# Kernel tuning notes

Hardware: AMD Instinct MI355X
Metric: run time of the kernel (lower is better)

The kernel has to match this reference:

```python
import jax, jax.numpy as jnp
import numpy as np

N = 12000   # nodes (multiple of 120)
E = 192000  # edges
T = 120     # utterances per dialogue
IN = 192
OUT = 6


def _edge_softmax(logits, dst, n):
    # logits: [E, H] -> softmax over incoming edges of each dst node
    m = jax.ops.segment_max(logits, dst, num_segments=n)
    ex = jnp.exp(logits - m[dst])
    s = jax.ops.segment_sum(ex, dst, num_segments=n)
    return ex / s[dst]


def _gatv2(h, src, dst, Wsrc, bsrc, Wdst, bdst, attn, Wres, n):
    # DGL GATv2Conv: e = attn . leakyrelu(fc_src(h)[u] + fc_dst(h)[v]), residual, relu activation
    Hh, F = attn.shape
    fs = (h @ Wsrc + bsrc).reshape(n, Hh, F)
    fd = (h @ Wdst + bdst).reshape(n, Hh, F)
    e = jax.nn.leaky_relu(fs[src] + fd[dst], 0.2)          # [E, H, F]
    logits = jnp.einsum('ehf,hf->eh', e, attn)              # [E, H]
    alpha = _edge_softmax(logits, dst, n)                   # [E, H]
    out = jax.ops.segment_sum(alpha[:, :, None] * fs[src], dst, num_segments=n)
    res = (h @ Wres).reshape(n, Hh, F)
    return jax.nn.relu(out + res)                           # [N, H, F]


def _lstm_dir(x, Wih, Whh, bih, bhh, reverse):
    # x: [T, B, D]; torch gate order i, f, g, o
    B = x.shape[1]
    hid = Whh.shape[1]
    def step(carry, xt):
        h, c = carry
        z = xt @ Wih.T + h @ Whh.T + bih + bhh
        i, f, g, o = jnp.split(z, 4, axis=-1)
        c = jax.nn.sigmoid(f) * c + jax.nn.sigmoid(i) * jnp.tanh(g)
        h = jax.nn.sigmoid(o) * jnp.tanh(c)
        return (h, c), h
    init = (jnp.zeros((B, hid), x.dtype), jnp.zeros((B, hid), x.dtype))
    _, hs = jax.lax.scan(step, init, x, reverse=reverse)
    return hs


def setup_inputs() -> dict:
    key = jax.random.key(0)
    ks = iter(jax.random.split(key, 64))
    def rn(shape, s=0.05):
        return jax.random.normal(next(ks), shape, jnp.float32) * s
    inp = {
        'text': rn((N, 1024), 1.0),
        'audio': rn((N, 512), 1.0),
        'vision': rn((N, 1024), 1.0),
        'edge_src': jax.random.randint(next(ks), (E,), 0, N, jnp.int32),
        'edge_dst': jax.random.randint(next(ks), (E,), 0, N, jnp.int32),
        # modality encoders
        'W_audio': rn((512, 64)), 'b_audio': jnp.zeros((64,), jnp.float32),
        'W_vision': rn((1024, 64)), 'b_vision': jnp.zeros((64,), jnp.float32),
        'W_text': rn((1024, 64)), 'b_text': jnp.zeros((64,), jnp.float32),
        # bidirectional LSTM (hidden=4 -> 16 gate rows)
        'Wih_f': rn((16, IN)), 'Whh_f': rn((16, 4)), 'bih_f': jnp.zeros((16,), jnp.float32), 'bhh_f': jnp.zeros((16,), jnp.float32),
        'Wih_b': rn((16, IN)), 'Whh_b': rn((16, 4)), 'bih_b': jnp.zeros((16,), jnp.float32), 'bhh_b': jnp.zeros((16,), jnp.float32),
        # imputation GraphConv (192->192, norm='both')
        'W_gc': rn((IN, IN)), 'b_gc': jnp.zeros((IN,), jnp.float32),
        # gat2 (cross-modal multi-head GAT, 192 -> 16 heads x 4)
        'Wsrc2': rn((IN, 64)), 'bsrc2': jnp.zeros((64,), jnp.float32),
        'Wdst2': rn((IN, 64)), 'bdst2': jnp.zeros((64,), jnp.float32),
        'attn2': rn((16, 4)), 'Wres2': rn((IN, 64)),
        # gat1 layer 0 (192 -> 16 heads x 32)
        'Wsrc0': rn((IN, 512)), 'bsrc0': jnp.zeros((512,), jnp.float32),
        'Wdst0': rn((IN, 512)), 'bdst0': jnp.zeros((512,), jnp.float32),
        'attn0': rn((16, 32)), 'Wres0': rn((IN, 512)),
        # gat1 layer 1 (512 -> 16 heads x 4)
        'Wsrc1': rn((512, 64)), 'bsrc1': jnp.zeros((64,), jnp.float32),
        'Wdst1': rn((512, 64)), 'bdst1': jnp.zeros((64,), jnp.float32),
        'attn1': rn((16, 4)), 'Wres1': rn((512, 64)),
        # final classifier Linear(136, out_size)
        'W_lin': rn((136, OUT)), 'b_lin': jnp.zeros((OUT,), jnp.float32),
    }
    return inp


def reference(text, audio, vision, edge_src, edge_dst,
              W_audio, b_audio, W_vision, b_vision, W_text, b_text,
              Wih_f, Whh_f, bih_f, bhh_f, Wih_b, Whh_b, bih_b, bhh_b,
              W_gc, b_gc,
              Wsrc2, bsrc2, Wdst2, bdst2, attn2, Wres2,
              Wsrc0, bsrc0, Wdst0, bdst0, attn0, Wres0,
              Wsrc1, bsrc1, Wdst1, bdst1, attn1, Wres1,
              W_lin, b_lin):
    n = text.shape[0]
    # modality encoders (dropout is identity at inference)
    t = text @ W_text + b_text
    a = audio @ W_audio + b_audio
    v = vision @ W_vision + b_vision
    stackFT = jnp.concatenate([t, a, v], axis=1)            # [N, 192]

    # bidirectional LSTM over dialogues of length T=120
    x = stackFT.reshape(-1, T, IN).transpose(1, 0, 2)       # [T, B, 192]
    hf = _lstm_dir(x, Wih_f, Whh_f, bih_f, bhh_f, False)
    hb = _lstm_dir(x, Wih_b, Whh_b, bih_b, bhh_b, True)
    newFeature = jnp.concatenate([hf, hb], -1).transpose(1, 0, 2).reshape(n, 8)

    # GraphConv imputation, norm='both' (degrees clamped to 1 as in DGL)
    ones = jnp.ones((edge_src.shape[0],), stackFT.dtype)
    deg_out = jnp.maximum(jax.ops.segment_sum(ones, edge_src, num_segments=n), 1.0)
    deg_in = jnp.maximum(jax.ops.segment_sum(ones, edge_dst, num_segments=n), 1.0)
    hw = (stackFT @ W_gc) * (deg_out ** -0.5)[:, None]
    h1 = jax.ops.segment_sum(hw[edge_src], edge_dst, num_segments=n) * (deg_in ** -0.5)[:, None] + b_gc
    h = 0.5 * (stackFT + h1)
    # F.normalize(h, p=1)
    h = h / jnp.maximum(jnp.sum(jnp.abs(h), axis=1, keepdims=True), 1e-12)

    # cross-modal multi-head GAT branch -> [N, 64]
    h3 = _gatv2(h, edge_src, edge_dst, Wsrc2, bsrc2, Wdst2, bdst2, attn2, Wres2, n).reshape(n, -1)

    # stacked GATv2 layers
    h = _gatv2(h, edge_src, edge_dst, Wsrc0, bsrc0, Wdst0, bdst0, attn0, Wres0, n).reshape(n, -1)  # [N, 512]
    h = _gatv2(h, edge_src, edge_dst, Wsrc1, bsrc1, Wdst1, bdst1, attn1, Wres1, n).reshape(n, -1)  # [N, 64]

    out = jnp.concatenate([h, newFeature, h3], axis=1) @ W_lin + b_lin  # [N, out_size]
    return out
```

## Files before the change

kernel.cpp:

```cpp
#include <hip/hip_runtime.h>

typedef __attribute__((ext_vector_type(8))) short short8;
typedef __attribute__((ext_vector_type(4))) float f32x4;
typedef _Float16 half8v __attribute__((ext_vector_type(8)));

__device__ __forceinline__ unsigned short f2bf(float f) {
    unsigned u = __float_as_uint(f);
    u += 0x7FFFu + ((u >> 16) & 1u);
    return (unsigned short)(u >> 16);
}
__device__ __forceinline__ float bf2f(unsigned short h) {
    return __uint_as_float((unsigned)h << 16);
}

template<int MF, int OUTMODE>
__global__ __launch_bounds__(256)
void gemm_v7(const unsigned short* __restrict__ A, const unsigned short* __restrict__ B,
             const float* __restrict__ bias, const float* __restrict__ rowscale,
             void* __restrict__ Cv, const float* __restrict__ fin_num,
             const float* __restrict__ fin_den,
             int M, int Nb, int K, int ldc)
{
    __shared__ alignas(16) unsigned short As[MF * 64 * 32];
    __shared__ alignas(16) unsigned short Bs[4 * 64 * 8];
    const int t = threadIdx.x;
    const int w = t >> 6, l = t & 63;
    const int r16 = l & 15, kg = l >> 4;
    const int row0 = blockIdx.x * (64 * MF);
    const int col0 = blockIdx.y * 64;
    const int bcol = t & 63, bkg = t >> 6;

    f32x4 acc[MF][4] = {};
    const short8 z8 = {0, 0, 0, 0, 0, 0, 0, 0};

    int srow[MF], sch[MF];
    bool va[MF];
    const unsigned short* aptr[MF];
#pragma unroll
    for (int it = 0; it < MF; ++it) {
        int idx = it * 256 + t;
        srow[it] = idx >> 2; sch[it] = idx & 3;
        int gm = row0 + srow[it];
        va[it] = gm < M;
        aptr[it] = A + (size_t)gm * K + sch[it] * 8;
    }
    const unsigned short* bptr = B + (size_t)(bkg * 8) * Nb + col0 + bcol;

    short8 pa[MF];
    unsigned short pbv[8];
#pragma unroll
    for (int it = 0; it < MF; ++it)
        pa[it] = va[it] ? *reinterpret_cast<const short8*>(aptr[it]) : z8;
#pragma unroll
    for (int j = 0; j < 8; ++j) pbv[j] = bptr[(size_t)j * Nb];

    for (int k0 = 0; k0 < K; k0 += 32) {
#pragma unroll
        for (int it = 0; it < MF; ++it)
            *reinterpret_cast<short8*>(&As[srow[it] * 32 + sch[it] * 8]) = pa[it];
        {
            short8 hv;
#pragma unroll
            for (int j = 0; j < 8; ++j) hv[j] = (short)pbv[j];
            *reinterpret_cast<short8*>(&Bs[bkg * 512 + bcol * 8]) = hv;
        }
        __syncthreads();
        if (k0 + 32 < K) {
#pragma unroll
            for (int it = 0; it < MF; ++it)
                pa[it] = va[it] ? *reinterpret_cast<const short8*>(aptr[it] + k0 + 32) : z8;
#pragma unroll
            for (int j = 0; j < 8; ++j) pbv[j] = bptr[(size_t)(k0 + 32 + j) * Nb];
        }
        short8 af[MF];
#pragma unroll
        for (int mi = 0; mi < MF; ++mi)
            af[mi] = *reinterpret_cast<const short8*>(&As[((w * MF + mi) * 16 + r16) * 32 + kg * 8]);
#pragma unroll
        for (int ni = 0; ni < 4; ++ni) {
            short8 bf = *reinterpret_cast<const short8*>(&Bs[kg * 512 + (ni * 16 + r16) * 8]);
#pragma unroll
            for (int mi = 0; mi < MF; ++mi)
                acc[mi][ni] = __builtin_amdgcn_mfma_f32_16x16x32_bf16(af[mi], bf, acc[mi][ni], 0, 0, 0);
        }
        __syncthreads();
    }
#pragma unroll
    for (int mi = 0; mi < MF; ++mi)
#pragma unroll
        for (int ni = 0; ni < 4; ++ni) {
            int col = col0 + ni * 16 + r16;
            float bv = bias ? bias[col] : 0.f;
#pragma unroll
            for (int r = 0; r < 4; ++r) {
                int gm = row0 + (w * MF + mi) * 16 + kg * 4 + r;
                if (gm < M) {
                    float val = acc[mi][ni][r] + bv;
                    if (rowscale) val *= rowscale[gm];
                    size_t idx = (size_t)gm * ldc + col;
                    if (OUTMODE == 0) {
                        ((float*)Cv)[idx] = val;
                    } else if (OUTMODE == 1) {
                        ((unsigned short*)Cv)[idx] = f2bf(val);
                    } else {
                        float d = fin_den[(size_t)gm * 16 + (col >> 5)];
                        float inv = (d > 0.f) ? __fdividef(1.f, d) : 0.f;
                        float o = fmaxf(fin_num[idx] * inv + val, 0.f);
                        ((unsigned short*)Cv)[idx] = f2bf(o);
                    }
                }
            }
        }
}

__global__ __launch_bounds__(256)
void enc_f16v2(const float* __restrict__ text, const float* __restrict__ audio, const float* __restrict__ vision,
               const _Float16* __restrict__ Wf16,
               const float* __restrict__ bt, const float* __restrict__ ba, const float* __restrict__ bv,
               float* __restrict__ Cf, unsigned short* __restrict__ Cb, int M)
{
    __shared__ alignas(16) _Float16 Af[32 * 64];
    __shared__ alignas(16) _Float16 Bf[8 * 64 * 8];
    const int z = blockIdx.z;
    const float* A  = (z == 0) ? text : (z == 1) ? audio : vision;
    const _Float16* W = Wf16 + ((z == 0) ? 0 : (z == 1) ? 65536 : 98304);
    const float* bb = (z == 0) ? bt : (z == 1) ? ba : bv;
    const int K = (z == 1) ? 512 : 1024;

    const int t = threadIdx.x;
    const int w = t >> 6, l = t & 63;
    const int r16 = l & 15, kg = l >> 4;
    const int row0 = blockIdx.x * 32;
    const int mi = w & 1;
    const int ncol0 = (w >> 1) * 32;
    const int arow = t >> 3, ac8 = t & 7;
    const int bcol = t & 63, bw = t >> 6;

    const float* ap = A + (size_t)(row0 + arow) * K + ac8 * 8;
    const _Float16* wp = W + (size_t)(bw * 16) * 64 + bcol;

    float4 pa0 = *reinterpret_cast<const float4*>(ap);
    float4 pa1 = *reinterpret_cast<const float4*>(ap + 4);
    _Float16 pb[16];
#pragma unroll
    for (int j = 0; j < 16; ++j) pb[j] = wp[(size_t)j * 64];

    f32x4 acc[2] = {};
    const int asw = ac8 ^ (arow & 7);
    for (int k0 = 0; k0 < K; k0 += 64) {
        {
            half8v av;
            av[0] = (_Float16)pa0.x; av[1] = (_Float16)pa0.y;
            av[2] = (_Float16)pa0.z; av[3] = (_Float16)pa0.w;
            av[4] = (_Float16)pa1.x; av[5] = (_Float16)pa1.y;
            av[6] = (_Float16)pa1.z; av[7] = (_Float16)pa1.w;
            *reinterpret_cast<half8v*>(&Af[arow * 64 + asw * 8]) = av;
            half8v b0, b1;
#pragma unroll
            for (int j = 0; j < 8; ++j) { b0[j] = pb[j]; b1[j] = pb[8 + j]; }
            *reinterpret_cast<half8v*>(&Bf[(bw * 2) * 512 + bcol * 8]) = b0;
            *reinterpret_cast<half8v*>(&Bf[(bw * 2 + 1) * 512 + bcol * 8]) = b1;
        }
        __syncthreads();
        if (k0 + 64 < K) {
            pa0 = *reinterpret_cast<const float4*>(ap + k0 + 64);
            pa1 = *reinterpret_cast<const float4*>(ap + k0 + 68);
#pragma unroll
            for (int j = 0; j < 16; ++j) pb[j] = wp[(size_t)(k0 + 64 + j) * 64];
        }
        const int row = mi * 16 + r16;
        half8v afA = *reinterpret_cast<const half8v*>(&Af[row * 64 + (kg ^ (row & 7)) * 8]);
        half8v afB = *reinterpret_cast<const half8v*>(&Af[row * 64 + ((kg + 4) ^ (row & 7)) * 8]);
#pragma unroll
        for (int ni = 0; ni < 2; ++ni) {
            int cx = (ncol0 + ni * 16 + r16) * 8;
            half8v bf0 = *reinterpret_cast<const half8v*>(&Bf[kg * 512 + cx]);
            half8v bf1 = *reinterpret_cast<const half8v*>(&Bf[(kg + 4) * 512 + cx]);
            acc[ni] = __builtin_amdgcn_mfma_f32_16x16x32_f16(afA, bf0, acc[ni], 0, 0, 0);
            acc[ni] = __builtin_amdgcn_mfma_f32_16x16x32_f16(afB, bf1, acc[ni], 0, 0, 0);
        }
        __syncthreads();
    }
#pragma unroll
    for (int ni = 0; ni < 2; ++ni) {
        int col = ncol0 + ni * 16 + r16;
        float bvv = bb[col];
#pragma unroll
        for (int r = 0; r < 4; ++r) {
            int gr = row0 + mi * 16 + kg * 4 + r;
            if (gr < M) {
                float val = acc[ni][r] + bvv;
                size_t idx = (size_t)gr * 192 + z * 64 + col;
                Cf[idx] = val;
                Cb[idx] = f2bf(val);
            }
        }
    }
}

__global__ void pack_all(const float* __restrict__ Wt, const float* __restrict__ Wa, const float* __restrict__ Wv,
                         const float* __restrict__ Wgc,
                         const float* __restrict__ Ws2, const float* __restrict__ Wd2, const float* __restrict__ Wr2,
                         const float* __restrict__ bs2, const float* __restrict__ bd2,
                         const float* __restrict__ Ws0, const float* __restrict__ Wd0,
                         const float* __restrict__ bs0, const float* __restrict__ bd0,
                         const float* __restrict__ Wr0,
                         const float* __restrict__ Ws1, const float* __restrict__ Wd1, const float* __restrict__ Wr1,
                         const float* __restrict__ bs1, const float* __restrict__ bd1,
                         _Float16* __restrict__ encW, unsigned short* __restrict__ Wall, float* __restrict__ ball)
{
    int gid = blockIdx.x * blockDim.x + threadIdx.x;
    if (gid < 163840) {
        float v = (gid < 65536) ? Wt[gid] : (gid < 98304) ? Wa[gid - 65536] : Wv[gid - 98304];
        encW[gid] = (_Float16)v;
    }
    if (gid < 36864) {
        Wall[gid] = f2bf(Wgc[gid]);
    } else if (gid < 73728) {
        int i = gid - 36864, k = i / 192, c = i - k * 192;
        float v = (c < 64) ? Ws2[k * 64 + c] : (c < 128) ? Wd2[k * 64 + c - 64] : Wr2[k * 64 + c - 128];
        Wall[gid] = f2bf(v);
    } else if (gid < 270336) {
        int i = gid - 73728, k = i >> 10, c = i & 1023;
        float v = (c < 512) ? Ws0[k * 512 + c] : Wd0[k * 512 + c - 512];
        Wall[gid] = f2bf(v);
    } else if (gid < 368640) {
        Wall[gid] = f2bf(Wr0[gid - 270336]);
    } else if (gid < 466944) {
        int i = gid - 368640, k = i / 192, c = i - k * 192;
        float v = (c < 64) ? Ws1[k * 64 + c] : (c < 128) ? Wd1[k * 64 + c - 64] : Wr1[k * 64 + c - 128];
        Wall[gid] = f2bf(v);
    } else if (gid < 468352) {
        int i = gid - 466944;
        float v;
        if (i < 192)       v = (i < 64) ? bs2[i] : (i < 128) ? bd2[i - 64] : 0.f;
        else if (i < 1216) { int j = i - 192; v = (j < 512) ? bs0[j] : bd0[j - 512]; }
        else               { int j = i - 1216; v = (j < 64) ? bs1[j] : (j < 128) ? bd1[j - 64] : 0.f; }
        ball[i] = v;
    }
}

__global__ void deg_kernel(const int* __restrict__ src, const int* __restrict__ dst,
                           int* degout, int* degin, int E)
{
    int e = blockIdx.x * blockDim.x + threadIdx.x;
    if (e < E) {
        atomicAdd(&degout[src[e]], 1);
        atomicAdd(&degin[dst[e]], 1);
    }
}

__global__ __launch_bounds__(1024)
void scan_kernel(const int* __restrict__ degin, int* __restrict__ rowstart, int n)
{
    __shared__ int part[1024];
    int t = threadIdx.x;
    int chunk = (n + 1023) / 1024;
    int s = 0;
    for (int i = 0; i < chunk; ++i) {
        int idx = t * chunk + i;
        if (idx < n) s += degin[idx];
    }
    part[t] = s;
    __syncthreads();
    for (int o = 1; o < 1024; o <<= 1) {
        int v = (t >= o) ? part[t - o] : 0;
        __syncthreads();
        part[t] += v;
        __syncthreads();
    }
    int run = (t > 0) ? part[t - 1] : 0;
    for (int i = 0; i < chunk; ++i) {
        int idx = t * chunk + i;
        if (idx < n) { rowstart[idx] = run; run += degin[idx]; }
    }
    if (t == 1023) rowstart[n] = part[1023];
}

__global__ void perm_kernel(const int* __restrict__ dst, const int* __restrict__ rowstart,
                            int* cursor, int* __restrict__ perm, int E)
{
    int e = blockIdx.x * blockDim.x + threadIdx.x;
    if (e < E) {
        int v = dst[e];
        int p = atomicAdd(&cursor[v], 1);
        perm[rowstart[v] + p] = e;
    }
}

__global__ void gather_src_kernel(const int* __restrict__ esrc, int* perm, int E)
{
    int i = blockIdx.x * blockDim.x + threadIdx.x;
    if (i < E) perm[i] = esrc[perm[i]];
}

__global__ void rs_kernel(const int* degout, const int* degin, float* rso, float* rsi, int n)
{
    int i = blockIdx.x * blockDim.x + threadIdx.x;
    if (i < n) {
        rso[i] = rsqrtf((float)max(degout[i], 1));
        rsi[i] = rsqrtf((float)max(degin[i], 1));
    }
}

__global__ void lstm_pre(const float* __restrict__ x, const float* __restrict__ Wf,
                         const float* __restrict__ Wb,
                         const float* bf1, const float* bf2, const float* bb1, const float* bb2,
                         float* __restrict__ xWf, float* __restrict__ xWb, int n)
{
    int gid = blockIdx.x * blockDim.x + threadIdx.x;
    if (gid >= n * 32) return;
    int nn = gid >> 5, r = gid & 31, d = r >> 4, j = r & 15;
    const float* W = (d ? Wb : Wf) + j * 192;
    const float* xr = x + (size_t)nn * 192;
    float s = 0.f;
#pragma unroll 4
    for (int k = 0; k < 192; k += 4) {
        float4 xv = *reinterpret_cast<const float4*>(xr + k);
        float4 wv = *reinterpret_cast<const float4*>(W + k);
        s += xv.x * wv.x + xv.y * wv.y + xv.z * wv.z + xv.w * wv.w;
    }
    s += d ? (bb1[j] + bb2[j]) : (bf1[j] + bf2[j]);
    int b = nn / 120, tt = nn - b * 120;
    (d ? xWb : xWf)[((size_t)b * 16 + j) * 120 + tt] = s;
}

__device__ __forceinline__ float fsigm(float x) { return __fdividef(1.f, 1.f + __expf(-x)); }
__device__ __forceinline__ float ftanh(float x) { return 1.f - __fdividef(2.f, __expf(2.f * x) + 1.f); }

template<int DIR>
__device__ void lstm_chain(const float* __restrict__ xw, const float* __restrict__ whh,
                           float* __restrict__ newF, int b)
{
    int j = threadIdx.x & 15;
    int k = j & 3;
    float4 w = *reinterpret_cast<const float4*>(whh + j * 4);
    const float* xp = xw + ((size_t)b * 16 + j) * 120;
    float h0 = 0.f, h1 = 0.f, h2 = 0.f, h3 = 0.f, cst = 0.f;
    int tb0 = DIR ? 108 : 0;
    float4 a0 = *reinterpret_cast<const float4*>(xp + tb0);
    float4 a1 = *reinterpret_cast<const float4*>(xp + tb0 + 4);
    float4 a2 = *reinterpret_cast<const float4*>(xp + tb0 + 8);
    for (int ch = 0; ch < 10; ++ch) {
        float4 b0 = a0, b1 = a1, b2 = a2;
        if (ch < 9) {
            int nt = DIR ? (96 - ch * 12) : (12 + ch * 12);
            b0 = *reinterpret_cast<const float4*>(xp + nt);
            b1 = *reinterpret_cast<const float4*>(xp + nt + 4);
            b2 = *reinterpret_cast<const float4*>(xp + nt + 8);
        }
        float zz[12] = {a0.x, a0.y, a0.z, a0.w, a1.x, a1.y, a1.z, a1.w, a2.x, a2.y, a2.z, a2.w};
        int tbase = DIR ? (108 - ch * 12) : (ch * 12);
#pragma unroll
        for (int ii = 0; ii < 12; ++ii) {
            int idx = DIR ? (11 - ii) : ii;
            float z = zz[idx] + ((w.x * h0 + w.y * h1) + (w.z * h2 + w.w * h3));
            float zi = __shfl(z, k, 16);
            float zf = __shfl(z, k + 4, 16);
            float zg = __shfl(z, k + 8, 16);
            float zo = __shfl(z, k + 12, 16);
            float ig = fsigm(zi), fg = fsigm(zf), gg = ftanh(zg), og = fsigm(zo);
            cst = fg * cst + ig * gg;
            float hn = og * ftanh(cst);
            h0 = __shfl(hn, 0, 16); h1 = __shfl(hn, 1, 16);
            h2 = __shfl(hn, 2, 16); h3 = __shfl(hn, 3, 16);
            if (j < 4) newF[((size_t)b * 120 + tbase + idx) * 8 + DIR * 4 + j] = hn;
        }
        a0 = b0; a1 = b1; a2 = b2;
    }
}

__global__ __launch_bounds__(64)
void lstm_seq2(const float* __restrict__ xWf, const float* __restrict__ xWb,
               const float* __restrict__ Whhf, const float* __restrict__ Whhb,
               float* __restrict__ newF, int B)
{
    int sub = threadIdx.x >> 4;
    int chain = blockIdx.x * 4 + sub;
    if (chain >= 2 * B) return;
    int d = chain / B;
    int b = chain - d * B;
    if (d == 0) lstm_chain<0>(xWf, Whhf, newF, b);
    else        lstm_chain<1>(xWb, Whhb, newF, b);
}

__global__ __launch_bounds__(256)
void gc_combine5(const float* __restrict__ stackFT, const unsigned short* __restrict__ hw,
                 const int* __restrict__ rowstart, const int* __restrict__ csrc,
                 const float* __restrict__ rs_in,
                 const float* __restrict__ b_gc, unsigned short* __restrict__ hB, int n)
{
    int v = blockIdx.x * 4 + (threadIdx.x >> 6);
    int l = threadIdx.x & 63;
    if (v >= n) return;
    int s0 = rowstart[v], s1 = rowstart[v + 1];
    float sum0 = 0.f, sum1 = 0.f, sum2 = 0.f;

    unsigned short a0 = 0, a1 = 0, a2 = 0, b0 = 0, b1 = 0, b2 = 0;
    auto LD = [&](int i, unsigned short& x0, unsigned short& x1, unsigned short& x2) {
        const unsigned short* hr = hw + (size_t)csrc[i] * 192 + l;
        x0 = hr[0]; x1 = hr[64]; x2 = hr[128];
    };
    int i = s0;
    if (i < s1) LD(i, a0, a1, a2);
    if (i + 1 < s1) LD(i + 1, b0, b1, b2);
    for (; i + 2 < s1; i += 2) {
        unsigned short n0, n1, n2, m0 = 0, m1 = 0, m2 = 0;
        LD(i + 2, n0, n1, n2);
        if (i + 3 < s1) LD(i + 3, m0, m1, m2);
        sum0 += bf2f(a0) + bf2f(b0);
        sum1 += bf2f(a1) + bf2f(b1);
        sum2 += bf2f(a2) + bf2f(b2);
        a0 = n0; a1 = n1; a2 = n2; b0 = m0; b1 = m1; b2 = m2;
    }
    if (i < s1) { sum0 += bf2f(a0); sum1 += bf2f(a1); sum2 += bf2f(a2); }
    if (i + 1 < s1) { sum0 += bf2f(b0); sum1 += bf2f(b1); sum2 += bf2f(b2); }

    float ri = rs_in[v];
    const float* sf = stackFT + (size_t)v * 192 + l;
    float v0 = 0.5f * (sf[0]   + sum0 * ri + b_gc[l]);
    float v1 = 0.5f * (sf[64]  + sum1 * ri + b_gc[l + 64]);
    float v2 = 0.5f * (sf[128] + sum2 * ri + b_gc[l + 128]);
    float r = fabsf(v0) + fabsf(v1) + fabsf(v2);
#pragma unroll
    for (int o = 32; o; o >>= 1) r += __shfl_xor(r, o);
    float inv = __fdividef(1.f, fmaxf(r, 1e-12f));
    unsigned short* hp = hB + (size_t)v * 192 + l;
    hp[0]   = f2bf(v0 * inv);
    hp[64]  = f2bf(v1 * inv);
    hp[128] = f2bf(v2 * inv);
}

__global__ __launch_bounds__(256)
void gat_edge4c(const unsigned short* __restrict__ base,
                const float* __restrict__ attn,
                const int* __restrict__ rowstart, const int* __restrict__ csrc,
                float* __restrict__ outp, int n)
{
    int v = blockIdx.x * 16 + (threadIdx.x >> 4);
    int l = threadIdx.x & 15;
    if (v >= n) return;
    float4 at = *reinterpret_cast<const float4*>(attn + l * 4);
    ushort4 fdu = *reinterpret_cast<const ushort4*>(base + (size_t)v * 192 + 64 + l * 4);
    float fd0 = bf2f(fdu.x), fd1 = bf2f(fdu.y), fd2 = bf2f(fdu.z), fd3 = bf2f(fdu.w);
    float ac0 = 0.f, ac1 = 0.f, ac2 = 0.f, ac3 = 0.f, dn = 0.f;
    int s0 = rowstart[v], s1 = rowstart[v + 1];

    auto LD = [&](int i) -> ushort4 {
        return *reinterpret_cast<const ushort4*>(base + (size_t)csrc[i] * 192 + l * 4);
    };
    auto ACC = [&](ushort4 su) {
        float s0f = bf2f(su.x), s1f = bf2f(su.y), s2f = bf2f(su.z), s3f = bf2f(su.w);
        float e0 = s0f + fd0; e0 = fmaxf(e0, 0.2f * e0);
        float e1 = s1f + fd1; e1 = fmaxf(e1, 0.2f * e1);
        float e2 = s2f + fd2; e2 = fmaxf(e2, 0.2f * e2);
        float e3 = s3f + fd3; e3 = fmaxf(e3, 0.2f * e3);
        float p = e0 * at.x + e1 * at.y + e2 * at.z + e3 * at.w;
        float ex = __expf(p);
        ac0 += ex * s0f; ac1 += ex * s1f; ac2 += ex * s2f; ac3 += ex * s3f;
        dn += ex;
    };
    const ushort4 zu = make_ushort4(0, 0, 0, 0);
    ushort4 c0 = zu, c1 = zu;
    int i = s0;
    if (i < s1) c0 = LD(i);
    if (i + 1 < s1) c1 = LD(i + 1);
    for (; i + 2 < s1; i += 2) {
        ushort4 n0 = LD(i + 2);
        ushort4 n1 = (i + 3 < s1) ? LD(i + 3) : zu;
        ACC(c0); ACC(c1);
        c0 = n0; c1 = n1;
    }
    if (i < s1) ACC(c0);
    if (i + 1 < s1) ACC(c1);

    ushort4 ru = *reinterpret_cast<const ushort4*>(base + (size_t)v * 192 + 128 + l * 4);
    float inv = (dn > 0.f) ? __fdividef(1.f, dn) : 0.f;
    float4 o;
    o.x = fmaxf(ac0 * inv + bf2f(ru.x), 0.f);
    o.y = fmaxf(ac1 * inv + bf2f(ru.y), 0.f);
    o.z = fmaxf(ac2 * inv + bf2f(ru.z), 0.f);
    o.w = fmaxf(ac3 * inv + bf2f(ru.w), 0.f);
    *reinterpret_cast<float4*>(outp + (size_t)v * 64 + l * 4) = o;
}

__global__ __launch_bounds__(256)
void gat_edge32b(const unsigned short* __restrict__ base,
                 const float* __restrict__ attn,
                 const int* __restrict__ rowstart, const int* __restrict__ csrc,
                 float* __restrict__ num, float* __restrict__ den, int n)
{
    int v = blockIdx.x * 4 + (threadIdx.x >> 6);
    int l = threadIdx.x & 63;
    if (v >= n) return;
    float at[8];
    {
        float4 aA = *reinterpret_cast<const float4*>(attn + l * 8);
        float4 aB = *reinterpret_cast<const float4*>(attn + l * 8 + 4);
        at[0] = aA.x; at[1] = aA.y; at[2] = aA.z; at[3] = aA.w;
        at[4] = aB.x; at[5] = aB.y; at[6] = aB.z; at[7] = aB.w;
    }
    float fd[8];
    {
        short8 fdu = *reinterpret_cast<const short8*>(base + (size_t)v * 1024 + 512 + l * 8);
#pragma unroll
        for (int j = 0; j < 8; ++j) fd[j] = bf2f((unsigned short)fdu[j]);
    }
    float acc[8] = {};
    float dn = 0.f;
    int s0 = rowstart[v], s1 = rowstart[v + 1];

    auto LD = [&](int i) -> short8 {
        return *reinterpret_cast<const short8*>(base + (size_t)csrc[i] * 1024 + l * 8);
    };
    auto ACC = [&](short8 su) {
        float sf[8];
        float p = 0.f;
#pragma unroll
        for (int j = 0; j < 8; ++j) {
            sf[j] = bf2f((unsigned short)su[j]);
            float e = sf[j] + fd[j];
            e = fmaxf(e, 0.2f * e);
            p += e * at[j];
        }
        p += __shfl_xor(p, 1, 4);
        p += __shfl_xor(p, 2, 4);
        float ex = __expf(p);
#pragma unroll
        for (int j = 0; j < 8; ++j) acc[j] += ex * sf[j];
        dn += ex;
    };
    const short8 z8 = {0, 0, 0, 0, 0, 0, 0, 0};
    short8 c0 = z8, c1 = z8;
    int i = s0;
    if (i < s1) c0 = LD(i);
    if (i + 1 < s1) c1 = LD(i + 1);
    for (; i + 2 < s1; i += 2) {
        short8 n0 = LD(i + 2);
        short8 n1 = (i + 3 < s1) ? LD(i + 3) : z8;
        ACC(c0); ACC(c1);
        c0 = n0; c1 = n1;
    }
    if (i < s1) ACC(c0);
    if (i + 1 < s1) ACC(c1);

    float* np = num + (size_t)v * 512 + l * 8;
    *reinterpret_cast<float4*>(np)     = make_float4(acc[0], acc[1], acc[2], acc[3]);
    *reinterpret_cast<float4*>(np + 4) = make_float4(acc[4], acc[5], acc[6], acc[7]);
    if ((l & 3) == 0) den[(size_t)v * 16 + (l >> 2)] = dn;
}

__global__ void final_lin(const float* __restrict__ h1, const float* __restrict__ newF,
                          const float* __restrict__ h3, const float* __restrict__ W,
                          const float* __restrict__ bias, float* __restrict__ out, int n)
{
    int gid = blockIdx.x * blockDim.x + threadIdx.x;
    if (gid >= n * 6) return;
    int v = gid / 6, o = gid - v * 6;
    float s = bias[o];
    const float* a = h1 + (size_t)v * 64;
#pragma unroll 8
    for (int r = 0; r < 64; ++r) s += a[r] * W[r * 6 + o];
    const float* b = newF + (size_t)v * 8;
#pragma unroll
    for (int r = 0; r < 8; ++r) s += b[r] * W[(64 + r) * 6 + o];
    const float* c = h3 + (size_t)v * 64;
#pragma unroll 8
    for (int r = 0; r < 64; ++r) s += c[r] * W[(72 + r) * 6 + o];
    out[gid] = s;
}

extern "C" void kernel_launch(void* const* d_in, const int* in_sizes, int n_in,
                              void* d_out, int out_size, void* d_ws, size_t ws_size,
                              hipStream_t stream)
{
    const float* text   = (const float*)d_in[0];
    const float* audio  = (const float*)d_in[1];
    const float* vision = (const float*)d_in[2];
    const int*   esrc   = (const int*)d_in[3];
    const int*   edst   = (const int*)d_in[4];
    const float* W_audio = (const float*)d_in[5];  const float* b_audio = (const float*)d_in[6];
    const float* W_vision= (const float*)d_in[7];  const float* b_vision= (const float*)d_in[8];
    const float* W_text  = (const float*)d_in[9];  const float* b_text  = (const float*)d_in[10];
    const float* Wih_f = (const float*)d_in[11]; const float* Whh_f = (const float*)d_in[12];
    const float* bih_f = (const float*)d_in[13]; const float* bhh_f = (const float*)d_in[14];
    const float* Wih_b = (const float*)d_in[15]; const float* Whh_b = (const float*)d_in[16];
    const float* bih_b = (const float*)d_in[17]; const float* bhh_b = (const float*)d_in[18];
    const float* W_gc  = (const float*)d_in[19]; const float* b_gc  = (const float*)d_in[20];
    const float* Wsrc2 = (const float*)d_in[21]; const float* bsrc2 = (const float*)d_in[22];
    const float* Wdst2 = (const float*)d_in[23]; const float* bdst2 = (const float*)d_in[24];
    const float* attn2 = (const float*)d_in[25]; const float* Wres2 = (const float*)d_in[26];
    const float* Wsrc0 = (const float*)d_in[27]; const float* bsrc0 = (const float*)d_in[28];
    const float* Wdst0 = (const float*)d_in[29]; const float* bdst0 = (const float*)d_in[30];
    const float* attn0 = (const float*)d_in[31]; const float* Wres0 = (const float*)d_in[32];
    const float* Wsrc1 = (const float*)d_in[33]; const float* bsrc1 = (const float*)d_in[34];
    const float* Wdst1 = (const float*)d_in[35]; const float* bdst1 = (const float*)d_in[36];
    const float* attn1 = (const float*)d_in[37]; const float* Wres1 = (const float*)d_in[38];
    const float* W_lin = (const float*)d_in[39]; const float* b_lin = (const float*)d_in[40];
    float* out = (float*)d_out;

    const int n = in_sizes[0] / 1024;
    const int E = in_sizes[3];
    const int B = n / 120;

    char* p = (char*)d_ws;
    auto alloc_f = [&](size_t cnt) { float* r = (float*)p; p += ((cnt * 4 + 255) / 256) * 256; return r; };
    auto alloc_h = [&](size_t cnt) { unsigned short* r = (unsigned short*)p; p += ((cnt * 2 + 255) / 256) * 256; return r; };
    auto alloc_i = [&](size_t cnt) { int* r = (int*)p; p += ((cnt * 4 + 255) / 256) * 256; return r; };
    float*          stackFT = alloc_f((size_t)n * 192);
    unsigned short* stackBF = alloc_h((size_t)n * 192);
    unsigned short* hbufBF  = alloc_h((size_t)n * 192);
    unsigned short* encW    = alloc_h(163840);
    float* xWf     = alloc_f((size_t)n * 16);
    float* xWb     = alloc_f((size_t)n * 16);
    float* newF    = alloc_f((size_t)n * 8);
    float* big0    = alloc_f((size_t)n * 512);
    float* big1    = alloc_f((size_t)n * 512);
    float* big2    = alloc_f((size_t)n * 512);
    float* den     = alloc_f((size_t)n * 16);
    float* h3      = alloc_f((size_t)n * 64);
    float* h1s     = alloc_f((size_t)n * 64);
    float* rs_out  = alloc_f(n);
    float* rs_in   = alloc_f(n);
    int* zero_base = alloc_i((size_t)3 * n);
    int* degout = zero_base;
    int* degin  = zero_base + n;
    int* cursor = zero_base + 2 * n;
    int* rowstart = alloc_i((size_t)n + 1);
    int* perm     = alloc_i((size_t)E);
    if ((size_t)(p - (char*)d_ws) > ws_size) return;

    unsigned short* Wall = (unsigned short*)h1s;
    float* ball = h1s + 240000;
    const unsigned short* Wp_gc = Wall;
    const unsigned short* Wp_g2 = Wall + 36864;
    const unsigned short* Wp_g0 = Wall + 73728;
    const unsigned short* Wp_r0 = Wall + 270336;
    const unsigned short* Wp_g1 = Wall + 368640;
    const float* bp_g2 = ball;
    const float* bp_g0 = ball + 192;
    const float* bp_g1 = ball + 1216;

    hipMemsetAsync(zero_base, 0, (size_t)3 * n * 4, stream);
    pack_all<<<(468352 + 255) / 256, 256, 0, stream>>>(
        W_text, W_audio, W_vision, W_gc,
        Wsrc2, Wdst2, Wres2, bsrc2, bdst2,
        Wsrc0, Wdst0, bsrc0, bdst0, Wres0,
        Wsrc1, Wdst1, Wres1, bsrc1, bdst1,
        (_Float16*)encW, Wall, ball);
    deg_kernel<<<(E + 255) / 256, 256, 0, stream>>>(esrc, edst, degout, degin, E);
    scan_kernel<<<1, 1024, 0, stream>>>(degin, rowstart, n);
    perm_kernel<<<(E + 255) / 256, 256, 0, stream>>>(edst, rowstart, cursor, perm, E);
    gather_src_kernel<<<(E + 255) / 256, 256, 0, stream>>>(esrc, perm, E);
    rs_kernel<<<(n + 255) / 256, 256, 0, stream>>>(degout, degin, rs_out, rs_in, n);
    const int* csrc = perm;

    auto gemm = [&](auto mf_tag, auto om_tag, const unsigned short* A, const unsigned short* Bm,
                    const float* bias, const float* rsc, void* Cp,
                    const float* fnum, const float* fden, int M, int Nb, int K, int ldc) {
        constexpr int MF = decltype(mf_tag)::value;
        constexpr int OM = decltype(om_tag)::value;
        dim3 grid((M + 64 * MF - 1) / (64 * MF), Nb / 64);
        gemm_v7<MF, OM><<<grid, 256, 0, stream>>>(A, Bm, bias, rsc, Cp, fnum, fden, M, Nb, K, ldc);
    };
    using I1 = std::integral_constant<int, 1>;
    using I2 = std::integral_constant<int, 2>;
    using O1 = std::integral_constant<int, 1>;
    using O2 = std::integral_constant<int, 2>;

    {
        dim3 grid(n / 32, 1, 3);
        enc_f16v2<<<grid, 256, 0, stream>>>(text, audio, vision, (const _Float16*)encW,
                                            b_text, b_audio, b_vision, stackFT, stackBF, n);
    }

    lstm_pre<<<(n * 32 + 255) / 256, 256, 0, stream>>>(stackFT, Wih_f, Wih_b,
                                                       bih_f, bhh_f, bih_b, bhh_b, xWf, xWb, n);
    lstm_seq2<<<(2 * B + 3) / 4, 64, 0, stream>>>(xWf, xWb, Whh_f, Whh_b, newF, B);

    gemm(I1{}, O1{}, stackBF, Wp_gc, nullptr, rs_out, big0, nullptr, nullptr, n, 192, 192, 192);
    gc_combine5<<<(n + 3) / 4, 256, 0, stream>>>(stackFT, (const unsigned short*)big0,
                                                 rowstart, csrc, rs_in, b_gc, hbufBF, n);

    gemm(I1{}, O1{}, hbufBF, Wp_g2, bp_g2, nullptr, big0, nullptr, nullptr, n, 192, 192, 192);
    gat_edge4c<<<(n + 15) / 16, 256, 0, stream>>>((const unsigned short*)big0, attn2, rowstart, csrc, h3, n);

    gemm(I2{}, O1{}, hbufBF, Wp_g0, bp_g0, nullptr, big0, nullptr, nullptr, n, 1024, 192, 1024);
    gat_edge32b<<<(n + 3) / 4, 256, 0, stream>>>((const unsigned short*)big0, attn0, rowstart, csrc, big2, den, n);
    gemm(I1{}, O2{}, hbufBF, Wp_r0, nullptr, nullptr, big1, big2, den, n, 512, 192, 512);

    gemm(I1{}, O1{}, (const unsigned short*)big1, Wp_g1, bp_g1, nullptr, big0, nullptr, nullptr, n, 192, 512, 192);
    gat_edge4c<<<(n + 15) / 16, 256, 0, stream>>>((const unsigned short*)big0, attn1, rowstart, csrc, h1s, n);

    final_lin<<<(n * 6 + 255) / 256, 256, 0, stream>>>(h1s, newF, h3, W_lin, b_lin, out, n);
}
```

Before: 344.2 us.

## Rewrite encoder GEMM as LDS-free per-wave MFMA with prepacked weight fragments

New measurement: 358.5 us. 1.04x slower.

```diff
diff --git a/kernel.cpp b/kernel.cpp
--- a/kernel.cpp
+++ b/kernel.cpp
@@ -114,86 +114,69 @@
 }
 
 __global__ __launch_bounds__(256)
-void enc_f16v2(const float* __restrict__ text, const float* __restrict__ audio, const float* __restrict__ vision,
+void enc_f16v5(const float* __restrict__ text, const float* __restrict__ audio, const float* __restrict__ vision,
                const _Float16* __restrict__ Wf16,
                const float* __restrict__ bt, const float* __restrict__ ba, const float* __restrict__ bv,
                float* __restrict__ Cf, unsigned short* __restrict__ Cb, int M)
 {
-    __shared__ alignas(16) _Float16 Af[32 * 64];
-    __shared__ alignas(16) _Float16 Bf[8 * 64 * 8];
-    const int z = blockIdx.z;
+    const int gw = (blockIdx.x * blockDim.x + threadIdx.x) >> 6;
+    const int l = threadIdx.x & 63;
+    const int tpm = M >> 4;
+    if (gw >= 3 * tpm) return;
+    const int z = gw / tpm;
+    const int tile = gw - z * tpm;
     const float* A  = (z == 0) ? text : (z == 1) ? audio : vision;
-    const _Float16* W = Wf16 + ((z == 0) ? 0 : (z == 1) ? 65536 : 98304);
+    const _Float16* Wp = Wf16 + ((z == 0) ? 0 : (z == 1) ? 65536 : 98304) + l * 8;
     const float* bb = (z == 0) ? bt : (z == 1) ? ba : bv;
-    const int K = (z == 1) ? 512 : 1024;
-
-    const int t = threadIdx.x;
-    const int w = t >> 6, l = t & 63;
-    const int r16 = l & 15, kg = l >> 4;
-    const int row0 = blockIdx.x * 32;
-    const int mi = w & 1;
-    const int ncol0 = (w >> 1) * 32;
-    const int arow = t >> 3, ac8 = t & 7;
-    const int bcol = t & 63, bw = t >> 6;
-
-    const float* ap = A + (size_t)(row0 + arow) * K + ac8 * 8;
-    const _Float16* wp = W + (size_t)(bw * 16) * 64 + bcol;
-
-    float4 pa0 = *reinterpret_cast<const float4*>(ap);
-    float4 pa1 = *reinterpret_cast<const float4*>(ap + 4);
-    _Float16 pb[16];
-#pragma unroll
-    for (int j = 0; j < 16; ++j) pb[j] = wp[(size_t)j * 64];
-
-    f32x4 acc[2] = {};
-    const int asw = ac8 ^ (arow & 7);
-    for (int k0 = 0; k0 < K; k0 += 64) {
-        {
-            half8v av;
-            av[0] = (_Float16)pa0.x; av[1] = (_Float16)pa0.y;
-            av[2] = (_Float16)pa0.z; av[3] = (_Float16)pa0.w;
-            av[4] = (_Float16)pa1.x; av[5] = (_Float16)pa1.y;
-            av[6] = (_Float16)pa1.z; av[7] = (_Float16)pa1.w;
-            *reinterpret_cast<half8v*>(&Af[arow * 64 + asw * 8]) = av;
-            half8v b0, b1;
-#pragma unroll
-            for (int j = 0; j < 8; ++j) { b0[j] = pb[j]; b1[j] = pb[8 + j]; }
-            *reinterpret_cast<half8v*>(&Bf[(bw * 2) * 512 + bcol * 8]) = b0;
-            *reinterpret_cast<half8v*>(&Bf[(bw * 2 + 1) * 512 + bcol * 8]) = b1;
-        }
-        __syncthreads();
-        if (k0 + 64 < K) {
-            pa0 = *reinterpret_cast<const float4*>(ap + k0 + 64);
-            pa1 = *reinterpret_cast<const float4*>(ap + k0 + 68);
-#pragma unroll
-            for (int j = 0; j < 16; ++j) pb[j] = wp[(size_t)(k0 + 64 + j) * 64];
-        }
-        const int row = mi * 16 + r16;
-        half8v afA = *reinterpret_cast<const half8v*>(&Af[row * 64 + (kg ^ (row & 7)) * 8]);
-        half8v afB = *reinterpret_cast<const half8v*>(&Af[row * 64 + ((kg + 4) ^ (row & 7)) * 8]);
-#pragma unroll
-        for (int ni = 0; ni < 2; ++ni) {
-            int cx = (ncol0 + ni * 16 + r16) * 8;
-            half8v bf0 = *reinterpret_cast<const half8v*>(&Bf[kg * 512 + cx]);
-            half8v bf1 = *reinterpret_cast<const half8v*>(&Bf[(kg + 4) * 512 + cx]);
-            acc[ni] = __builtin_amdgcn_mfma_f32_16x16x32_f16(afA, bf0, acc[ni], 0, 0, 0);
-            acc[ni] = __builtin_amdgcn_mfma_f32_16x16x32_f16(afB, bf1, acc[ni], 0, 0, 0);
-        }
-        __syncthreads();
-    }
-#pragma unroll
-    for (int ni = 0; ni < 2; ++ni) {
-        int col = ncol0 + ni * 16 + r16;
+    const int KC = (z == 1) ? 16 : 32;
+
+    const float* ap = A + (size_t)(tile * 16 + (l & 15)) * (KC * 32) + (l >> 4) * 8;
+
+    f32x4 acc0 = {}, acc1 = {}, acc2 = {}, acc3 = {};
+    float4 na0 = *reinterpret_cast<const float4*>(ap);
+    float4 na1 = *reinterpret_cast<const float4*>(ap + 4);
+    half8v nb0 = *reinterpret_cast<const half8v*>(Wp);
+    half8v nb1 = *reinterpret_cast<const half8v*>(Wp + 512);
+    half8v nb2 = *reinterpret_cast<const half8v*>(Wp + 1024);
+    half8v nb3 = *reinterpret_cast<const half8v*>(Wp + 1536);
+
+    for (int kc = 0; kc < KC; ++kc) {
+        float4 ca0 = na0, ca1 = na1;
+        half8v cb0 = nb0, cb1 = nb1, cb2 = nb2, cb3 = nb3;
+        if (kc + 1 < KC) {
+            const float* apn = ap + (kc + 1) * 32;
+            na0 = *reinterpret_cast<const float4*>(apn);
+            na1 = *reinterpret_cast<const float4*>(apn + 4);
+            const _Float16* wpn = Wp + (size_t)(kc + 1) * 2048;
+            nb0 = *reinterpret_cast<const half8v*>(wpn);
+            nb1 = *reinterpret_cast<const half8v*>(wpn + 512);
+            nb2 = *reinterpret_cast<const half8v*>(wpn + 1024);
+            nb3 = *reinterpret_cast<const half8v*>(wpn + 1536);
+        }
+        half8v af;
+        af[0] = (_Float16)ca0.x; af[1] = (_Float16)ca0.y;
+        af[2] = (_Float16)ca0.z; af[3] = (_Float16)ca0.w;
+        af[4] = (_Float16)ca1.x; af[5] = (_Float16)ca1.y;
+        af[6] = (_Float16)ca1.z; af[7] = (_Float16)ca1.w;
+        acc0 = __builtin_amdgcn_mfma_f32_16x16x32_f16(af, cb0, acc0, 0, 0, 0);
+        acc1 = __builtin_amdgcn_mfma_f32_16x16x32_f16(af, cb1, acc1, 0, 0, 0);
+        acc2 = __builtin_amdgcn_mfma_f32_16x16x32_f16(af, cb2, acc2, 0, 0, 0);
+        acc3 = __builtin_amdgcn_mfma_f32_16x16x32_f16(af, cb3, acc3, 0, 0, 0);
+    }
+
+    const int r16 = l & 15, hi = l >> 4;
+#pragma unroll
+    for (int cg = 0; cg < 4; ++cg) {
+        f32x4 a = (cg == 0) ? acc0 : (cg == 1) ? acc1 : (cg == 2) ? acc2 : acc3;
+        int col = cg * 16 + r16;
         float bvv = bb[col];
 #pragma unroll
         for (int r = 0; r < 4; ++r) {
-            int gr = row0 + mi * 16 + kg * 4 + r;
-            if (gr < M) {
-                float val = acc[ni][r] + bvv;
-                size_t idx = (size_t)gr * 192 + z * 64 + col;
-                Cf[idx] = val;
-                Cb[idx] = f2bf(val);
-            }
+            int row = tile * 16 + hi * 4 + r;
+            size_t idx = (size_t)row * 192 + z * 64 + col;
+            float val = a[r] + bvv;
+            Cf[idx] = val;
+            Cb[idx] = f2bf(val);
         }
     }
 }
@@ -211,8 +194,17 @@
 {
     int gid = blockIdx.x * blockDim.x + threadIdx.x;
     if (gid < 163840) {
-        float v = (gid < 65536) ? Wt[gid] : (gid < 98304) ? Wa[gid - 65536] : Wv[gid - 98304];
-        encW[gid] = (_Float16)v;
+        const float* Wsrcp;
+        int base;
+        if (gid < 65536)      { base = 0;     Wsrcp = Wt; }
+        else if (gid < 98304) { base = 65536; Wsrcp = Wa; }
+        else                  { base = 98304; Wsrcp = Wv; }
+        int i = gid - base;
+        int kc = i >> 11, r = i & 2047;
+        int cg = r >> 9, lane = (r >> 3) & 63, j = r & 7;
+        int k = kc * 32 + (lane >> 4) * 8 + j;
+        int col = cg * 16 + (lane & 15);
+        encW[gid] = (_Float16)Wsrcp[k * 64 + col];
     }
     if (gid < 36864) {
         Wall[gid] = f2bf(Wgc[gid]);
@@ -251,7 +243,8 @@
 }
 
 __global__ __launch_bounds__(1024)
-void scan_kernel(const int* __restrict__ degin, int* __restrict__ rowstart, int n)
+void scan_kernel(const int* __restrict__ degin, const int* __restrict__ degout,
+                 int* __restrict__ rowstart, float* __restrict__ rso, float* __restrict__ rsi, int n)
 {
     __shared__ int part[1024];
     int t = threadIdx.x;
@@ -272,7 +265,11 @@
     int run = (t > 0) ? part[t - 1] : 0;
     for (int i = 0; i < chunk; ++i) {
         int idx = t * chunk + i;
-        if (idx < n) { rowstart[idx] = run; run += degin[idx]; }
+        if (idx < n) {
+            rowstart[idx] = run; run += degin[idx];
+            rso[idx] = rsqrtf((float)max(degout[idx], 1));
+            rsi[idx] = rsqrtf((float)max(degin[idx], 1));
+        }
     }
     if (t == 1023) rowstart[n] = part[1023];
 }
@@ -292,15 +289,6 @@
 {
     int i = blockIdx.x * blockDim.x + threadIdx.x;
     if (i < E) perm[i] = esrc[perm[i]];
-}
-
-__global__ void rs_kernel(const int* degout, const int* degin, float* rso, float* rsi, int n)
-{
-    int i = blockIdx.x * blockDim.x + threadIdx.x;
-    if (i < n) {
-        rso[i] = rsqrtf((float)max(degout[i], 1));
-        rsi[i] = rsqrtf((float)max(degin[i], 1));
-    }
 }
 
 __global__ void lstm_pre(const float* __restrict__ x, const float* __restrict__ Wf,
@@ -649,10 +637,9 @@
         Wsrc1, Wdst1, Wres1, bsrc1, bdst1,
         (_Float16*)encW, Wall, ball);
     deg_kernel<<<(E + 255) / 256, 256, 0, stream>>>(esrc, edst, degout, degin, E);
-    scan_kernel<<<1, 1024, 0, stream>>>(degin, rowstart, n);
+    scan_kernel<<<1, 1024, 0, stream>>>(degin, degout, rowstart, rs_out, rs_in, n);
     perm_kernel<<<(E + 255) / 256, 256, 0, stream>>>(edst, rowstart, cursor, perm, E);
     gather_src_kernel<<<(E + 255) / 256, 256, 0, stream>>>(esrc, perm, E);
-    rs_kernel<<<(n + 255) / 256, 256, 0, stream>>>(degout, degin, rs_out, rs_in, n);
     const int* csrc = perm;
 
     auto gemm = [&](auto mf_tag, auto om_tag, const unsigned short* A, const unsigned short* Bm,
@@ -669,9 +656,10 @@
     using O2 = std::integral_constant<int, 2>;
 
     {
-        dim3 grid(n / 32, 1, 3);
-        enc_f16v2<<<grid, 256, 0, stream>>>(text, audio, vision, (const _Float16*)encW,
-                                            b_text, b_audio, b_vision, stackFT, stackBF, n);
+        int waves = 3 * (n >> 4);
+        enc_f16v5<<<(waves * 64 + 255) / 256, 256, 0, stream>>>(
+            text, audio, vision, (const _Float16*)encW,
+            b_text, b_audio, b_vision, stackFT, stackBF, n);
     }
 
     lstm_pre<<<(n * 32 + 255) / 256, 256, 0, stream>>>(stackFT, Wih_f, Wih_b,
```
